# Optimization experiments

Hardware: AMD Instinct MI355X
Metric: run time of the kernel (lower is better)

Reference implementation:

```python
import jax, jax.numpy as jnp
import numpy as np

B, T, I, H, O = 256, 2048, 6, 64, 6  # batch, time, input_dim, hidden_dim, output_dim


def setup_inputs() -> dict:
    key = jax.random.key(0)
    ks = jax.random.split(key, 11)
    s = 0.1  # param init scale
    return {
        "x": jax.random.normal(ks[0], (B, T, I), jnp.float32),
        # LSTM layer 0 (gate order i, f, g, o as in PyTorch; b = b_ih + b_hh)
        "Wih0": jax.random.normal(ks[1], (4 * H, I), jnp.float32) * s,
        "Whh0": jax.random.normal(ks[2], (4 * H, H), jnp.float32) * s,
        "b0": jax.random.normal(ks[3], (4 * H,), jnp.float32) * s,
        # LSTM layer 1
        "Wih1": jax.random.normal(ks[4], (4 * H, H), jnp.float32) * s,
        "Whh1": jax.random.normal(ks[5], (4 * H, H), jnp.float32) * s,
        "b1": jax.random.normal(ks[6], (4 * H,), jnp.float32) * s,
        # FC head
        "W1": jax.random.normal(ks[7], (H, H), jnp.float32) * s,
        "bf1": jax.random.normal(ks[8], (H,), jnp.float32) * s,
        "W2": jax.random.normal(ks[9], (O, H), jnp.float32) * s,
        "bf2": jax.random.normal(ks[10], (O,), jnp.float32) * s,
    }


def lstm_layer(x, Wih, Whh, b):
    """Single LSTM layer, batch_first. x: (B, T, F) -> (B, T, H)."""
    h_dim = Whh.shape[1]
    # precompute input contribution to gates for all timesteps: (B, T, 4H)
    xg = jnp.einsum('btf,gf->btg', x, Wih) + b

    def step(carry, xg_t):
        h, c = carry
        g = xg_t + h @ Whh.T                      # (B, 4H)
        i, f, gg, o = jnp.split(g, 4, axis=-1)    # PyTorch gate order i,f,g,o
        i = jax.nn.sigmoid(i)
        f = jax.nn.sigmoid(f)
        gg = jnp.tanh(gg)
        o = jax.nn.sigmoid(o)
        c = f * c + i * gg
        h = o * jnp.tanh(c)
        return (h, c), h

    h0 = jnp.zeros((x.shape[0], h_dim), x.dtype)
    _, hs = jax.lax.scan(step, (h0, h0), jnp.swapaxes(xg, 0, 1))  # (T, B, H)
    return jnp.swapaxes(hs, 0, 1)


def reference(x, Wih0, Whh0, b0, Wih1, Whh1, b1, W1, bf1, W2, bf2):
    h = lstm_layer(x, Wih0, Whh0, b0)
    h = lstm_layer(h, Wih1, Whh1, b1)   # eval mode: inter-layer dropout disabled
    h = jax.nn.relu(h @ W1.T + bf1)
    return h @ W2.T + bf2               # (B, T, O)
```

## Files before the change

### kernel.cpp

```cpp
#include <hip/hip_runtime.h>

#define TT 2048
#define HH 64
#define II 6
#define OO 6
#define NTHR 512

typedef float    f32x4 __attribute__((ext_vector_type(4)));
typedef float    f32x2 __attribute__((ext_vector_type(2)));
typedef _Float16 f16x8 __attribute__((ext_vector_type(8)));

__device__ __forceinline__ float fast_sig(float v) {
    return __builtin_amdgcn_rcpf(1.0f + __expf(-v));
}
__device__ __forceinline__ float fast_tanh(float v) {
    return 1.0f - 2.0f * __builtin_amdgcn_rcpf(__expf(2.0f * v) + 1.0f);
}

#define MFMA(a, b, c) __builtin_amdgcn_mfma_f32_16x16x32_f16((a), (b), (c), 0, 0, 0)

#define LGKM_BARRIER() asm volatile("s_waitcnt lgkmcnt(0)\ns_barrier" ::: "memory")

__global__
__attribute__((amdgpu_flat_work_group_size(NTHR, NTHR)))
__attribute__((amdgpu_waves_per_eu(2, 2)))
void lstm_mfma_kernel(const float* __restrict__ x,
                      const float* __restrict__ Wih0, const float* __restrict__ Whh0,
                      const float* __restrict__ b0,
                      const float* __restrict__ Wih1, const float* __restrict__ Whh1,
                      const float* __restrict__ b1,
                      const float* __restrict__ W1, const float* __restrict__ bf1,
                      const float* __restrict__ W2, const float* __restrict__ bf2,
                      float* __restrict__ out)
{
    const int row  = blockIdx.x;
    const int tid  = threadIdx.x;
    const int wid  = tid >> 6;
    const int lane = tid & 63;
    const int n    = lane & 15;
    const int q    = lane >> 4;
    const bool isA = wid < 4;
    const int  w   = isA ? wid : wid - 4;

    __shared__ __attribute__((aligned(16))) _Float16 H0[2][HH];
    __shared__ __attribute__((aligned(16))) _Float16 H1[2][HH];
    __shared__ __attribute__((aligned(16))) _Float16 Rb[2][HH];
    __shared__ __attribute__((aligned(16))) float    XG[2][256];

    if (tid < HH) {
        H0[0][tid] = (_Float16)0.f; H0[1][tid] = (_Float16)0.f;
        H1[0][tid] = (_Float16)0.f; H1[1][tid] = (_Float16)0.f;
        Rb[0][tid] = (_Float16)0.f; Rb[1][tid] = (_Float16)0.f;
    }
    if (tid < 256) { XG[0][tid] = 0.f; XG[1][tid] = 0.f; }

    f16x8 frag[20];
    float bias[8];
    #pragma unroll
    for (int i = 0; i < 8; ++i) bias[i] = 0.f;

    auto mk = [&](const float* W, int r, int ld, int kbase, int kmax, bool rok) {
        f16x8 f;
        #pragma unroll
        for (int i = 0; i < 8; ++i) {
            int kk = kbase + 8 * q + i;
            f[i] = (rok && kk < kmax) ? (_Float16)W[r * ld + kk] : (_Float16)0.f;
        }
        return f;
    };

    if (isA) {
        #pragma unroll
        for (int g = 0; g < 4; ++g) {
            const int r0 = g * HH + 16 * w + n;
            frag[g * 3 + 0] = mk(Whh0, r0, HH, 0,  HH, true);
            frag[g * 3 + 1] = mk(Whh0, r0, HH, 32, HH, true);
            frag[g * 3 + 2] = mk(Wih0, r0, II, 0,  II, true);
            bias[g] = b0[r0];
            const int r1 = 16 * (4 * g + w) + n;
            frag[12 + g * 2 + 0] = mk(Wih1, r1, HH, 0,  HH, true);
            frag[12 + g * 2 + 1] = mk(Wih1, r1, HH, 32, HH, true);
            bias[4 + g] = b1[r1];
        }
    } else {
        #pragma unroll
        for (int g = 0; g < 4; ++g) {
            const int r0 = g * HH + 16 * w + n;
            frag[g * 2 + 0] = mk(Whh1, r0, HH, 0,  HH, true);
            frag[g * 2 + 1] = mk(Whh1, r0, HH, 32, HH, true);
        }
        const int rf = 16 * w + n;
        frag[8]  = mk(W1, rf, HH, 0,  HH, true);
        frag[9]  = mk(W1, rf, HH, 32, HH, true);
        bias[0] = bf1[rf];
        frag[10] = mk(W2, n, HH, 0,  HH, n < OO);
        frag[11] = mk(W2, n, HH, 32, HH, n < OO);
        bias[1] = (n < OO) ? bf2[n] : 0.f;
        #pragma unroll
        for (int i = 12; i < 20; ++i) frag[i] = frag[0];
    }

    const float* xrow = x + (size_t)row * TT * II;
    {
        unsigned long long p = (unsigned long long)xrow;
        asm volatile("" : "+v"(p));
        xrow = (const float*)p;
    }
    f32x4 xc03 = {0.f, 0.f, 0.f, 0.f};
    f32x2 xc45 = {0.f, 0.f};
    if (isA) {
        xc03 = *reinterpret_cast<const f32x4*>(xrow);
        xc45 = *reinterpret_cast<const f32x2*>(xrow + 4);
    }

    float* outrow = out + (size_t)row * TT * OO;
    float cst = 0.f;

    __syncthreads();

    for (int t = 0; t <= TT + 3; ++t) {
        const int slp = (t + 1) & 1;
        const int slc = t & 1;

        if (isA) {
            const int tn = (t + 1 < TT) ? t + 1 : TT - 1;
            const float* xp = xrow + (size_t)tn * II;
            f32x4 xn03 = *reinterpret_cast<const f32x4*>(xp);
            f32x2 xn45 = *reinterpret_cast<const f32x2*>(xp + 4);

            const f16x8 a0 = *reinterpret_cast<const f16x8*>(&H0[slp][8 * q]);
            const f16x8 a1 = *reinterpret_cast<const f16x8*>(&H0[slp][32 + 8 * q]);
            f16x8 a2;
            a2[0] = (_Float16)xc03[0]; a2[1] = (_Float16)xc03[1];
            a2[2] = (_Float16)xc03[2]; a2[3] = (_Float16)xc03[3];
            a2[4] = (_Float16)xc45[0]; a2[5] = (_Float16)xc45[1];
            a2[6] = (_Float16)0.f;     a2[7] = (_Float16)0.f;

            f32x4 d0, d1, d2, d3;
            #pragma unroll
            for (int g = 0; g < 4; ++g) {
                f32x4 acc = {bias[g], bias[g], bias[g], bias[g]};
                acc = MFMA(a0, frag[g * 3 + 0], acc);
                acc = MFMA(a1, frag[g * 3 + 1], acc);
                acc = MFMA(a2, frag[g * 3 + 2], acc);
                if (g == 0) d0 = acc; else if (g == 1) d1 = acc;
                else if (g == 2) d2 = acc; else d3 = acc;
                f32x4 ae = {bias[4 + g], bias[4 + g], bias[4 + g], bias[4 + g]};
                ae = MFMA(a0, frag[12 + g * 2 + 0], ae);
                ae = MFMA(a1, frag[12 + g * 2 + 1], ae);
                if (lane < 16) XG[slp][16 * (4 * g + w) + lane] = ae[0];
            }
            if (t < TT) {
                float i_ = fast_sig(d0[0]), f_ = fast_sig(d1[0]);
                float g_ = fast_tanh(d2[0]), o_ = fast_sig(d3[0]);
                cst = f_ * cst + i_ * g_;
                float h = o_ * fast_tanh(cst);
                if (lane < 16) H0[slc][16 * w + lane] = (_Float16)h;
            }
            xc03 = xn03;
            xc45 = xn45;
        } else {
            const int s2 = t - 2, s3 = t - 3, s4 = t - 4;
            const f16x8 a0 = *reinterpret_cast<const f16x8*>(&H1[slp][8 * q]);
            const f16x8 a1 = *reinterpret_cast<const f16x8*>(&H1[slp][32 + 8 * q]);
            f32x4 d0, d1, d2, d3;
            #pragma unroll
            for (int g = 0; g < 4; ++g) {
                const float xg = XG[slc][16 * (4 * g + w) + n];
                f32x4 acc = {xg, xg, xg, xg};
                acc = MFMA(a0, frag[g * 2 + 0], acc);
                acc = MFMA(a1, frag[g * 2 + 1], acc);
                if (g == 0) d0 = acc; else if (g == 1) d1 = acc;
                else if (g == 2) d2 = acc; else d3 = acc;
            }
            if (s2 >= 0 && s2 < TT) {
                float i_ = fast_sig(d0[0]), f_ = fast_sig(d1[0]);
                float g_ = fast_tanh(d2[0]), o_ = fast_sig(d3[0]);
                cst = f_ * cst + i_ * g_;
                float h = o_ * fast_tanh(cst);
                if (lane < 16) H1[slc][16 * w + lane] = (_Float16)h;
            }
            {
                f32x4 acc = {bias[0], bias[0], bias[0], bias[0]};
                acc = MFMA(a0, frag[8], acc);
                acc = MFMA(a1, frag[9], acc);
                if (s3 >= 0 && s3 < TT && lane < 16)
                    Rb[slp][16 * w + lane] = (_Float16)fmaxf(acc[0], 0.f);
            }
            if (w == 0) {
                const f16x8 r0 = *reinterpret_cast<const f16x8*>(&Rb[slc][8 * q]);
                const f16x8 r1 = *reinterpret_cast<const f16x8*>(&Rb[slc][32 + 8 * q]);
                f32x4 acc = {bias[1], bias[1], bias[1], bias[1]};
                acc = MFMA(r0, frag[10], acc);
                acc = MFMA(r1, frag[11], acc);
                if (s4 >= 0 && s4 < TT && lane < OO)
                    outrow[(size_t)s4 * OO + lane] = acc[0];
            }
        }
        LGKM_BARRIER();
    }
}

extern "C" void kernel_launch(void* const* d_in, const int* in_sizes, int n_in,
                              void* d_out, int out_size, void* d_ws, size_t ws_size,
                              hipStream_t stream) {
    const float* xp   = (const float*)d_in[0];
    const float* Wih0 = (const float*)d_in[1];
    const float* Whh0 = (const float*)d_in[2];
    const float* b0   = (const float*)d_in[3];
    const float* Wih1 = (const float*)d_in[4];
    const float* Whh1 = (const float*)d_in[5];
    const float* b1   = (const float*)d_in[6];
    const float* W1   = (const float*)d_in[7];
    const float* bf1  = (const float*)d_in[8];
    const float* W2   = (const float*)d_in[9];
    const float* bf2  = (const float*)d_in[10];
    float* outp = (float*)d_out;

    lstm_mfma_kernel<<<dim3(256), dim3(NTHR), 0, stream>>>(
        xp, Wih0, Whh0, b0, Wih1, Whh1, b1, W1, bf1, W2, bf2, outp);
}
```

Baseline: 1.235 ms.

## Move layer-1 input projection into B waves and FC1 into A waves

Layer-1's input projection (Wih1·h0) now runs in the layer-1 waves, which read h0 straight from a 4-deep H0 ring. This removes the fp32 XG shared-memory staging. The FC1 ReLU projection moves from the layer-1 waves to the layer-0 waves, which balances the MFMA count per step (A: 14, B: 16+2) and takes the XG stores and loads off the critical path. The trade-off is two extra MFMAs on the serial layer-1 chain and more LDS ring slots to keep the skewed timesteps consistent.

```diff
diff --git a/kernel.cpp b/kernel.cpp
--- a/kernel.cpp
+++ b/kernel.cpp
@@ -42,22 +42,16 @@
     const bool isA = wid < 4;
     const int  w   = isA ? wid : wid - 4;
 
-    __shared__ __attribute__((aligned(16))) _Float16 H0[2][HH];
+    __shared__ __attribute__((aligned(16))) _Float16 H0[4][HH];
     __shared__ __attribute__((aligned(16))) _Float16 H1[2][HH];
     __shared__ __attribute__((aligned(16))) _Float16 Rb[2][HH];
-    __shared__ __attribute__((aligned(16))) float    XG[2][256];
 
     if (tid < HH) {
         H0[0][tid] = (_Float16)0.f; H0[1][tid] = (_Float16)0.f;
+        H0[2][tid] = (_Float16)0.f; H0[3][tid] = (_Float16)0.f;
         H1[0][tid] = (_Float16)0.f; H1[1][tid] = (_Float16)0.f;
         Rb[0][tid] = (_Float16)0.f; Rb[1][tid] = (_Float16)0.f;
     }
-    if (tid < 256) { XG[0][tid] = 0.f; XG[1][tid] = 0.f; }
-
-    f16x8 frag[20];
-    float bias[8];
-    #pragma unroll
-    for (int i = 0; i < 8; ++i) bias[i] = 0.f;
 
     auto mk = [&](const float* W, int r, int ld, int kbase, int kmax, bool rok) {
         f16x8 f;
@@ -68,6 +62,10 @@
         }
         return f;
     };
+    auto splat = [](float v) { f32x4 r = {v, v, v, v}; return r; };
+
+    f16x8 frag[16], fragX[2];
+    f32x4 biasv[4], biasX;
 
     if (isA) {
         #pragma unroll
@@ -76,28 +74,27 @@
             frag[g * 3 + 0] = mk(Whh0, r0, HH, 0,  HH, true);
             frag[g * 3 + 1] = mk(Whh0, r0, HH, 32, HH, true);
             frag[g * 3 + 2] = mk(Wih0, r0, II, 0,  II, true);
-            bias[g] = b0[r0];
-            const int r1 = 16 * (4 * g + w) + n;
-            frag[12 + g * 2 + 0] = mk(Wih1, r1, HH, 0,  HH, true);
-            frag[12 + g * 2 + 1] = mk(Wih1, r1, HH, 32, HH, true);
-            bias[4 + g] = b1[r1];
-        }
+            biasv[g] = splat(b0[r0]);
+        }
+        const int rf = 16 * w + n;
+        fragX[0] = mk(W1, rf, HH, 0,  HH, true);
+        fragX[1] = mk(W1, rf, HH, 32, HH, true);
+        biasX = splat(bf1[rf]);
+        #pragma unroll
+        for (int i = 12; i < 16; ++i) frag[i] = frag[0];
     } else {
         #pragma unroll
         for (int g = 0; g < 4; ++g) {
             const int r0 = g * HH + 16 * w + n;
-            frag[g * 2 + 0] = mk(Whh1, r0, HH, 0,  HH, true);
-            frag[g * 2 + 1] = mk(Whh1, r0, HH, 32, HH, true);
-        }
-        const int rf = 16 * w + n;
-        frag[8]  = mk(W1, rf, HH, 0,  HH, true);
-        frag[9]  = mk(W1, rf, HH, 32, HH, true);
-        bias[0] = bf1[rf];
-        frag[10] = mk(W2, n, HH, 0,  HH, n < OO);
-        frag[11] = mk(W2, n, HH, 32, HH, n < OO);
-        bias[1] = (n < OO) ? bf2[n] : 0.f;
-        #pragma unroll
-        for (int i = 12; i < 20; ++i) frag[i] = frag[0];
+            frag[g * 4 + 0] = mk(Wih1, r0, HH, 0,  HH, true);
+            frag[g * 4 + 1] = mk(Wih1, r0, HH, 32, HH, true);
+            frag[g * 4 + 2] = mk(Whh1, r0, HH, 0,  HH, true);
+            frag[g * 4 + 3] = mk(Whh1, r0, HH, 32, HH, true);
+            biasv[g] = splat(b1[r0]);
+        }
+        fragX[0] = mk(W2, n, HH, 0,  HH, n < OO);
+        fragX[1] = mk(W2, n, HH, 32, HH, n < OO);
+        biasX = splat((n < OO) ? bf2[n] : 0.f);
     }
 
     const float* xrow = x + (size_t)row * TT * II;
@@ -119,8 +116,8 @@
     __syncthreads();
 
     for (int t = 0; t <= TT + 3; ++t) {
-        const int slp = (t + 1) & 1;
-        const int slc = t & 1;
+        const int slp2 = (t + 1) & 1;
+        const int slc2 = t & 1;
 
         if (isA) {
             const int tn = (t + 1 < TT) ? t + 1 : TT - 1;
@@ -128,8 +125,8 @@
             f32x4 xn03 = *reinterpret_cast<const f32x4*>(xp);
             f32x2 xn45 = *reinterpret_cast<const f32x2*>(xp + 4);
 
-            const f16x8 a0 = *reinterpret_cast<const f16x8*>(&H0[slp][8 * q]);
-            const f16x8 a1 = *reinterpret_cast<const f16x8*>(&H0[slp][32 + 8 * q]);
+            const f16x8 a0 = *reinterpret_cast<const f16x8*>(&H0[(t + 3) & 3][8 * q]);
+            const f16x8 a1 = *reinterpret_cast<const f16x8*>(&H0[(t + 3) & 3][32 + 8 * q]);
             f16x8 a2;
             a2[0] = (_Float16)xc03[0]; a2[1] = (_Float16)xc03[1];
             a2[2] = (_Float16)xc03[2]; a2[3] = (_Float16)xc03[3];
@@ -139,37 +136,43 @@
             f32x4 d0, d1, d2, d3;
             #pragma unroll
             for (int g = 0; g < 4; ++g) {
-                f32x4 acc = {bias[g], bias[g], bias[g], bias[g]};
-                acc = MFMA(a0, frag[g * 3 + 0], acc);
+                f32x4 acc = MFMA(a0, frag[g * 3 + 0], biasv[g]);
                 acc = MFMA(a1, frag[g * 3 + 1], acc);
                 acc = MFMA(a2, frag[g * 3 + 2], acc);
                 if (g == 0) d0 = acc; else if (g == 1) d1 = acc;
                 else if (g == 2) d2 = acc; else d3 = acc;
-                f32x4 ae = {bias[4 + g], bias[4 + g], bias[4 + g], bias[4 + g]};
-                ae = MFMA(a0, frag[12 + g * 2 + 0], ae);
-                ae = MFMA(a1, frag[12 + g * 2 + 1], ae);
-                if (lane < 16) XG[slp][16 * (4 * g + w) + lane] = ae[0];
             }
             if (t < TT) {
                 float i_ = fast_sig(d0[0]), f_ = fast_sig(d1[0]);
                 float g_ = fast_tanh(d2[0]), o_ = fast_sig(d3[0]);
                 cst = f_ * cst + i_ * g_;
                 float h = o_ * fast_tanh(cst);
-                if (lane < 16) H0[slc][16 * w + lane] = (_Float16)h;
+                if (lane < 16) H0[t & 3][16 * w + lane] = (_Float16)h;
+            }
+            {
+                const int s3 = t - 3;
+                const f16x8 b0f = *reinterpret_cast<const f16x8*>(&H1[slp2][8 * q]);
+                const f16x8 b1f = *reinterpret_cast<const f16x8*>(&H1[slp2][32 + 8 * q]);
+                f32x4 acc = MFMA(b0f, fragX[0], biasX);
+                acc = MFMA(b1f, fragX[1], acc);
+                if (s3 >= 0 && s3 < TT && lane < 16)
+                    Rb[slp2][16 * w + lane] = (_Float16)fmaxf(acc[0], 0.f);
             }
             xc03 = xn03;
             xc45 = xn45;
         } else {
-            const int s2 = t - 2, s3 = t - 3, s4 = t - 4;
-            const f16x8 a0 = *reinterpret_cast<const f16x8*>(&H1[slp][8 * q]);
-            const f16x8 a1 = *reinterpret_cast<const f16x8*>(&H1[slp][32 + 8 * q]);
+            const int s2 = t - 2, s4 = t - 4;
+            const f16x8 h00 = *reinterpret_cast<const f16x8*>(&H0[(t + 2) & 3][8 * q]);
+            const f16x8 h01 = *reinterpret_cast<const f16x8*>(&H0[(t + 2) & 3][32 + 8 * q]);
+            const f16x8 a0  = *reinterpret_cast<const f16x8*>(&H1[slp2][8 * q]);
+            const f16x8 a1  = *reinterpret_cast<const f16x8*>(&H1[slp2][32 + 8 * q]);
             f32x4 d0, d1, d2, d3;
             #pragma unroll
             for (int g = 0; g < 4; ++g) {
-                const float xg = XG[slc][16 * (4 * g + w) + n];
-                f32x4 acc = {xg, xg, xg, xg};
-                acc = MFMA(a0, frag[g * 2 + 0], acc);
-                acc = MFMA(a1, frag[g * 2 + 1], acc);
+                f32x4 acc = MFMA(h00, frag[g * 4 + 0], biasv[g]);
+                acc = MFMA(h01, frag[g * 4 + 1], acc);
+                acc = MFMA(a0,  frag[g * 4 + 2], acc);
+                acc = MFMA(a1,  frag[g * 4 + 3], acc);
                 if (g == 0) d0 = acc; else if (g == 1) d1 = acc;
                 else if (g == 2) d2 = acc; else d3 = acc;
             }
@@ -178,21 +181,13 @@
                 float g_ = fast_tanh(d2[0]), o_ = fast_sig(d3[0]);
                 cst = f_ * cst + i_ * g_;
                 float h = o_ * fast_tanh(cst);
-                if (lane < 16) H1[slc][16 * w + lane] = (_Float16)h;
-            }
-            {
-                f32x4 acc = {bias[0], bias[0], bias[0], bias[0]};
-                acc = MFMA(a0, frag[8], acc);
-                acc = MFMA(a1, frag[9], acc);
-                if (s3 >= 0 && s3 < TT && lane < 16)
-                    Rb[slp][16 * w + lane] = (_Float16)fmaxf(acc[0], 0.f);
+                if (lane < 16) H1[slc2][16 * w + lane] = (_Float16)h;
             }
             if (w == 0) {
-                const f16x8 r0 = *reinterpret_cast<const f16x8*>(&Rb[slc][8 * q]);
-                const f16x8 r1 = *reinterpret_cast<const f16x8*>(&Rb[slc][32 + 8 * q]);
-                f32x4 acc = {bias[1], bias[1], bias[1], bias[1]};
-                acc = MFMA(r0, frag[10], acc);
-                acc = MFMA(r1, frag[11], acc);
+                const f16x8 r0 = *reinterpret_cast<const f16x8*>(&Rb[slc2][8 * q]);
+                const f16x8 r1 = *reinterpret_cast<const f16x8*>(&Rb[slc2][32 + 8 * q]);
+                f32x4 acc = MFMA(r0, fragX[0], biasX);
+                acc = MFMA(r1, fragX[1], acc);
                 if (s4 >= 0 && s4 < TT && lane < OO)
                     outrow[(size_t)s4 * OO + lane] = acc[0];
             }
```

New measurement: 1.360 ms. +10.1%, slower.
